# Performance work log

Measured on AMD Instinct MI355X. Metric: run time of the kernel, lower is better.

## Reference

```python
import jax, jax.numpy as jnp
import numpy as np

B, C, H, W = 16, 256, 32, 32
N_HEAD, DIM_HEAD = 8, 32  # dim_hidden = 256 == C


def setup_inputs() -> dict:
    key = jax.random.key(0)
    ks = jax.random.split(key, 9)
    s = 1.0 / np.sqrt(C)
    return {
        "x": jax.random.normal(ks[0], (B, C, H, W), dtype=jnp.float32),
        "w_q": jax.random.normal(ks[1], (C, C), dtype=jnp.float32) * s,
        "b_q": jnp.zeros((C,), dtype=jnp.float32),
        "w_k": jax.random.normal(ks[2], (C, C), dtype=jnp.float32) * s,
        "b_k": jnp.zeros((C,), dtype=jnp.float32),
        "w_v": jax.random.normal(ks[3], (C, C), dtype=jnp.float32) * s,
        "b_v": jnp.zeros((C,), dtype=jnp.float32),
        "w_o": jax.random.normal(ks[4], (C, C), dtype=jnp.float32) * s,
        "b_o": jnp.zeros((C,), dtype=jnp.float32),
    }


def reference(x, w_q, b_q, w_k, b_k, w_v, b_v, w_o, b_o):
    b, c, h, w = x.shape
    L = h * w
    scale = DIM_HEAD ** (-0.5)
    xf = x.reshape(b, c, L)  # [b, c, L]

    def proj(wm, bm):
        # 1x1 conv == per-position linear over channels
        y = jnp.einsum('oc,bcl->bol', wm, xf) + bm[None, :, None]
        return y.reshape(b, N_HEAD, DIM_HEAD, L)

    q = proj(w_q, b_q) * scale
    k = proj(w_k, b_k)
    v = proj(w_v, b_v)

    sim = jnp.einsum('bndl,bndm->bnlm', q, k)           # [b, n, L, L]
    att = jax.nn.softmax(sim, axis=-1)
    out = jnp.einsum('bnlm,bndm->bndl', att, v)         # [b, n, d, L]
    out = out.reshape(b, c, L)
    out = jnp.einsum('oc,bcl->bol', w_o, out) + b_o[None, :, None]
    return out.reshape(b, c, h, w)
```

## Files before the change

### kernel.cpp

```cpp
#include <hip/hip_runtime.h>
#include <hip/hip_bf16.h>
#include <math.h>

namespace {
constexpr int B_ = 16, C_ = 256, L_ = 1024, NH_ = 8, DH_ = 32;

typedef __attribute__((ext_vector_type(8))) short short8v;
typedef __attribute__((ext_vector_type(4))) float float4v;

__device__ __forceinline__ short f2bf(float f) {
    unsigned u = __builtin_bit_cast(unsigned, f);
    u += 0x7fffu + ((u >> 16) & 1u);
    return (short)(u >> 16);
}
__device__ __forceinline__ float bf2f(short s) {
    unsigned u = ((unsigned)(unsigned short)s) << 16;
    return __builtin_bit_cast(float, u);
}
__device__ __forceinline__ unsigned pkrn(float a, float b) {
    float2 f; f.x = a; f.y = b;
    __hip_bfloat162 h = __float22bfloat162_rn(f);
    unsigned u;
    __builtin_memcpy(&u, &h, sizeof(u));
    return u;
}
__device__ __forceinline__ void gld16(const short* g, short* l) {
    __builtin_amdgcn_global_load_lds(
        (const __attribute__((address_space(1))) unsigned*)g,
        (__attribute__((address_space(3))) unsigned*)l, 16, 0, 0);
}

__global__ __launch_bounds__(256) void xpose_kernel(
    const float* __restrict__ x, short* __restrict__ xthi)
{
    const int lt = blockIdx.x, ct = blockIdx.y, b = blockIdx.z;
    const int t = threadIdx.x;
    __shared__ float sX[64][68];

#pragma unroll
    for (int e = 0; e < 4; ++e) {
        const int row = e * 16 + (t >> 4);
        const int col = (t & 15) * 4;
        float4 v = *(const float4*)&x[((size_t)b * C_ + ct * 64 + row) * L_ + lt * 64 + col];
        *(float4*)&sX[row][col] = v;
    }
    __syncthreads();

    const int l = t & 63, cg = t >> 6;
    short hi[16];
#pragma unroll
    for (int i = 0; i < 16; ++i) hi[i] = f2bf(sX[cg * 16 + i][l]);
    const size_t base = ((size_t)b * L_ + lt * 64 + l) * C_ + ct * 64 + cg * 16;
    *(short8v*)&xthi[base]     = *(short8v*)&hi[0];
    *(short8v*)&xthi[base + 8] = *(short8v*)&hi[8];
}

__global__ __launch_bounds__(256) void stackw_kernel(
    const float* __restrict__ wq, const float* __restrict__ wk,
    const float* __restrict__ wv, const float* __restrict__ wo,
    short* __restrict__ WA, short* __restrict__ WoA)
{
    const int g = blockIdx.x * 256 + threadIdx.x;
    if (g < 768 * 256) {
        const int o = g >> 8, cc = g & 255;
        const float* src = (o < 256) ? wq : (o < 512) ? wk : wv;
        const float v = src[(size_t)(o & 255) * 256 + cc];
        const short hi = f2bf(v);
        const short lo = f2bf(v - bf2f(hi));
        WA[(size_t)o * 512 + cc]       = hi;
        WA[(size_t)o * 512 + 256 + cc] = lo;
    } else {
        const int g2 = g - 768 * 256;
        const int o = g2 >> 8, cc = g2 & 255;
        const float v = wo[(size_t)o * 256 + cc];
        const short hi = f2bf(v);
        const short lo = f2bf(v - bf2f(hi));
        WoA[(size_t)o * 512 + cc]       = hi;
        WoA[(size_t)o * 512 + 256 + cc] = lo;
    }
}

template <int KTOT, int EPI>
__global__ __launch_bounds__(256, 3) void gemm_kernel(
    const short* __restrict__ A, const short* __restrict__ B0,
    const float* __restrict__ bias0, const float* __restrict__ bias1, const float* __restrict__ bias2,
    float qscale, void* __restrict__ out0, void* __restrict__ out1, void* __restrict__ out2)
{
    const int lt = blockIdx.x, ot = blockIdx.y, b = blockIdx.z;
    const int t = threadIdx.x, wv = t >> 6, lane = t & 63;
    const int quad = lane >> 4, c = lane & 15;
    const int wo = (wv & 1) * 64, wl = (wv >> 1) * 64;

    __shared__ short sA[128 * 64];
    __shared__ short sB[128 * 64];

    float4v acc[4][4];
#pragma unroll
    for (int i = 0; i < 4; ++i)
#pragma unroll
        for (int j = 0; j < 4; ++j) acc[i][j] = (float4v)0.f;

    const short* Arow = A + (size_t)(ot * 128) * KTOT;
    const int srow = t >> 3, sseg = t & 7;
    const int seg = sseg ^ (srow & 7);

    for (int kk = 0; kk < KTOT / 64; ++kk) {
        __syncthreads();
#pragma unroll
        for (int e = 0; e < 4; ++e) {
            gld16(Arow + (size_t)(e * 32 + srow) * KTOT + kk * 64 + seg * 8,
                  &sA[(e * 256 + t) * 8]);
            gld16(B0 + ((size_t)b * L_ + lt * 128 + e * 32 + srow) * 256 + (kk & 3) * 64 + seg * 8,
                  &sB[(e * 256 + t) * 8]);
        }
        __syncthreads();

#pragma unroll
        for (int kc2 = 0; kc2 < 2; ++kc2) {
            short8v af[4], bf[4];
#pragma unroll
            for (int i = 0; i < 4; ++i) {
                const int row = wo + 16 * i + c;
                af[i] = *(const short8v*)&sA[row * 64 + (((kc2 * 4 + quad) ^ (c & 7)) * 8)];
            }
#pragma unroll
            for (int j = 0; j < 4; ++j) {
                const int row = wl + 16 * j + c;
                bf[j] = *(const short8v*)&sB[row * 64 + (((kc2 * 4 + quad) ^ (c & 7)) * 8)];
            }
#pragma unroll
            for (int i = 0; i < 4; ++i)
#pragma unroll
                for (int j = 0; j < 4; ++j)
                    acc[i][j] = __builtin_amdgcn_mfma_f32_16x16x32_bf16(af[i], bf[j], acc[i][j], 0, 0, 0);
        }
    }

    if constexpr (EPI == 0) {
        const int typ = ot >> 1;
        const int chbase = (ot & 1) * 128 + wo;
        const float* bp = (typ == 0) ? bias0 : (typ == 1) ? bias1 : bias2;
        const float sc = (typ == 0) ? qscale : 1.f;
        short* outp = (short*)((typ == 0) ? out0 : (typ == 1) ? out1 : out2);
        if (typ < 2) {
#pragma unroll
            for (int i = 0; i < 4; ++i) {
                const int ch0 = chbase + 16 * i + quad * 4;
                const int head = ch0 >> 5, d0 = ch0 & 31;
                float bias[4];
#pragma unroll
                for (int r = 0; r < 4; ++r) bias[r] = bp[ch0 + r];
#pragma unroll
                for (int j = 0; j < 4; ++j) {
                    const int l = lt * 128 + wl + 16 * j + c;
                    short4 sv;
                    sv.x = f2bf((acc[i][j][0] + bias[0]) * sc);
                    sv.y = f2bf((acc[i][j][1] + bias[1]) * sc);
                    sv.z = f2bf((acc[i][j][2] + bias[2]) * sc);
                    sv.w = f2bf((acc[i][j][3] + bias[3]) * sc);
                    *(short4*)&outp[(((size_t)b * NH_ + head) * L_ + l) * 32 + d0] = sv;
                }
            }
        } else {
#pragma unroll
            for (int i = 0; i < 4; ++i)
#pragma unroll
                for (int r = 0; r < 4; ++r) {
                    const int ch = chbase + 16 * i + quad * 4 + r;
                    const float bias = bp[ch];
#pragma unroll
                    for (int j = 0; j < 4; ++j)
                        outp[((size_t)b * C_ + ch) * L_ + lt * 128 + wl + 16 * j + c] =
                            f2bf(acc[i][j][r] + bias);
                }
        }
    } else {
        float* outp = (float*)out0;
#pragma unroll
        for (int i = 0; i < 4; ++i)
#pragma unroll
            for (int r = 0; r < 4; ++r) {
                const int ch = ot * 128 + wo + 16 * i + quad * 4 + r;
                const float bias = bias0[ch];
#pragma unroll
                for (int j = 0; j < 4; ++j)
                    outp[((size_t)b * C_ + ch) * L_ + lt * 128 + wl + 16 * j + c] =
                        acc[i][j][r] + bias;
            }
    }
}

__global__ __launch_bounds__(256, 4) void attn_kernel(
    const short* __restrict__ qt,
    const short* __restrict__ kt,
    const short* __restrict__ vb,
    short* __restrict__ athi)
{
    const int flat = blockIdx.x;
    const int g = ((flat >> 6) << 3) | (flat & 7);
    const int chunk = (flat >> 3) & 7;
    const int b = g >> 3, h = g & 7;
    const int t = threadIdx.x;
    const int wv = t >> 6, lane = t & 63;
    const int quad = lane >> 4, c = lane & 15;
    const int lq0 = chunk * 128 + wv * 32;

    __shared__ __align__(16) short sK[2][64 * 32];
    __shared__ __align__(16) short sV[2][2][32 * 32];
    __shared__ __align__(16) short sPT[4][2][16][72];

    const size_t bh = (size_t)b * NH_ + h;
    const short* qbase = qt + (bh * L_) * 32;
    const short* kbase = kt + (bh * L_) * 32;
    const size_t vrow = (size_t)b * C_ + h * DH_;

    short8v qfrag[2];
#pragma unroll
    for (int qf = 0; qf < 2; ++qf)
        qfrag[qf] = *(const short8v*)(qbase + (size_t)(lq0 + qf * 16 + c) * 32 + quad * 8);

    float lp4[2][4];
#pragma unroll
    for (int qf = 0; qf < 2; ++qf)
#pragma unroll
        for (int r = 0; r < 4; ++r) lp4[qf][r] = 0.f;
    float4v o_acc[2][2];
#pragma unroll
    for (int qf = 0; qf < 2; ++qf) { o_acc[qf][0] = (float4v)0.f; o_acc[qf][1] = (float4v)0.f; }

    auto stage = [&](int m0, int buf) {
        gld16(kbase + (size_t)(m0 + (t >> 2)) * 32 + (t & 3) * 8, &sK[buf][t * 8]);
        gld16(vb + (vrow + ((t >> 2) & 31)) * L_ + m0 + (t >> 7) * 32 + (t & 3) * 8,
              (short*)sV[buf] + t * 8);
    };

    stage(0, 0);

    for (int i = 0; i < 16; ++i) {
        __syncthreads();
        if (i < 15) stage((i + 1) * 64, (i + 1) & 1);
        const int buf = i & 1;

        short8v kf[4], vf[2][2];
#pragma unroll
        for (int kb = 0; kb < 4; ++kb)
            kf[kb] = *(const short8v*)&sK[buf][(kb * 16 + c) * 32 + quad * 8];
#pragma unroll
        for (int kc = 0; kc < 2; ++kc)
#pragma unroll
            for (int nb2 = 0; nb2 < 2; ++nb2)
                vf[kc][nb2] = *(const short8v*)&sV[buf][kc][(nb2 * 16 + c) * 32 + quad * 8];

        float4v st[2][4];
#pragma unroll
        for (int qf = 0; qf < 2; ++qf)
#pragma unroll
            for (int kb = 0; kb < 4; ++kb)
                st[qf][kb] = __builtin_amdgcn_mfma_f32_16x16x32_bf16(kf[kb], qfrag[qf], (float4v)0.f, 0, 0, 0);

#pragma unroll
        for (int qf = 0; qf < 2; ++qf)
#pragma unroll
            for (int kb = 0; kb < 4; ++kb) {
                float p[4];
#pragma unroll
                for (int r = 0; r < 4; ++r) {
                    p[r] = __builtin_amdgcn_exp2f(st[qf][kb][r]);
                    lp4[qf][r] += p[r];
                }
                uint2 w;
                w.x = pkrn(p[0], p[1]);
                w.y = pkrn(p[2], p[3]);
                *(uint2*)&sPT[wv][qf][c][kb * 16 + quad * 4] = w;
            }

#pragma unroll
        for (int qf = 0; qf < 2; ++qf)
#pragma unroll
            for (int kc = 0; kc < 2; ++kc) {
                const short8v pf = *(const short8v*)&sPT[wv][qf][c][kc * 32 + quad * 8];
#pragma unroll
                for (int nb2 = 0; nb2 < 2; ++nb2)
                    o_acc[qf][nb2] = __builtin_amdgcn_mfma_f32_16x16x32_bf16(vf[kc][nb2], pf, o_acc[qf][nb2], 0, 0, 0);
            }
    }

#pragma unroll
    for (int qf = 0; qf < 2; ++qf) {
        float l = (lp4[qf][0] + lp4[qf][1]) + (lp4[qf][2] + lp4[qf][3]);
        l += __shfl_xor(l, 16);
        l += __shfl_xor(l, 32);
        const float inv = 1.f / l;
#pragma unroll
        for (int nb2 = 0; nb2 < 2; ++nb2) {
            short4 sv;
            sv.x = f2bf(o_acc[qf][nb2][0] * inv);
            sv.y = f2bf(o_acc[qf][nb2][1] * inv);
            sv.z = f2bf(o_acc[qf][nb2][2] * inv);
            sv.w = f2bf(o_acc[qf][nb2][3] * inv);
            *(short4*)&athi[((size_t)b * L_ + lq0 + qf * 16 + c) * C_ + h * DH_ + nb2 * 16 + quad * 4] = sv;
        }
    }
}

}

extern "C" void kernel_launch(void* const* d_in, const int* in_sizes, int n_in,
                              void* d_out, int out_size, void* d_ws, size_t ws_size,
                              hipStream_t stream) {
    const float* x   = (const float*)d_in[0];
    const float* w_q = (const float*)d_in[1];
    const float* b_q = (const float*)d_in[2];
    const float* w_k = (const float*)d_in[3];
    const float* b_k = (const float*)d_in[4];
    const float* w_v = (const float*)d_in[5];
    const float* b_v = (const float*)d_in[6];
    const float* w_o = (const float*)d_in[7];
    const float* b_o = (const float*)d_in[8];
    float* out = (float*)d_out;

    const size_t NT = (size_t)B_ * L_ * C_;
    short* xthi = (short*)d_ws;
    short* WA   = xthi + NT;
    short* WoA  = WA + 768 * 512;
    short* qt   = WoA + 256 * 512;
    short* kt   = qt + NT;
    short* vb   = kt + NT;
    short* athi = vb + NT;

    const float scale_q = 0.17677669529663687f * 1.4426950408889634f;

    xpose_kernel<<<dim3(L_ / 64, C_ / 64, B_), 256, 0, stream>>>(x, xthi);
    stackw_kernel<<<dim3(1024), 256, 0, stream>>>(w_q, w_k, w_v, w_o, WA, WoA);
    gemm_kernel<512, 0><<<dim3(L_ / 128, 6, B_), 256, 0, stream>>>(
        WA, xthi, b_q, b_k, b_v, scale_q, qt, kt, vb);
    attn_kernel<<<dim3(1024), 256, 0, stream>>>(qt, kt, vb, athi);
    gemm_kernel<512, 1><<<dim3(L_ / 128, 2, B_), 256, 0, stream>>>(
        WoA, athi, b_o, nullptr, nullptr, 1.f, out, nullptr, nullptr);
}
```

Baseline: 151.3 us.

## Fuse x transpose/convert into QKV GEMM and software-pipeline attention PV step

Removes the separate transpose kernel: the QKV GEMM now reads fp32 x directly, converts it to bf16 and writes it transposed into padded shared memory. This saves one write and one read of a bf16 copy of x plus a kernel launch. The attention kernel is restructured so the P·V MFMA of the previous tile overlaps the QK/exp of the current one. It does this with a double-buffered, XOR-swizzled P buffer and single-buffered K/V with two barriers per step. The trade-offs are non-async global loads in the GEMM, which redo the conversion once per output tile, and extra synchronisation in attention.

```diff
diff --git a/kernel.cpp b/kernel.cpp
--- a/kernel.cpp
+++ b/kernel.cpp
@@ -28,31 +28,6 @@
     __builtin_amdgcn_global_load_lds(
         (const __attribute__((address_space(1))) unsigned*)g,
         (__attribute__((address_space(3))) unsigned*)l, 16, 0, 0);
-}
-
-__global__ __launch_bounds__(256) void xpose_kernel(
-    const float* __restrict__ x, short* __restrict__ xthi)
-{
-    const int lt = blockIdx.x, ct = blockIdx.y, b = blockIdx.z;
-    const int t = threadIdx.x;
-    __shared__ float sX[64][68];
-
-#pragma unroll
-    for (int e = 0; e < 4; ++e) {
-        const int row = e * 16 + (t >> 4);
-        const int col = (t & 15) * 4;
-        float4 v = *(const float4*)&x[((size_t)b * C_ + ct * 64 + row) * L_ + lt * 64 + col];
-        *(float4*)&sX[row][col] = v;
-    }
-    __syncthreads();
-
-    const int l = t & 63, cg = t >> 6;
-    short hi[16];
-#pragma unroll
-    for (int i = 0; i < 16; ++i) hi[i] = f2bf(sX[cg * 16 + i][l]);
-    const size_t base = ((size_t)b * L_ + lt * 64 + l) * C_ + ct * 64 + cg * 16;
-    *(short8v*)&xthi[base]     = *(short8v*)&hi[0];
-    *(short8v*)&xthi[base + 8] = *(short8v*)&hi[8];
 }
 
 __global__ __launch_bounds__(256) void stackw_kernel(
@@ -80,9 +55,9 @@
     }
 }
 
-template <int KTOT, int EPI>
+template <int EPI>
 __global__ __launch_bounds__(256, 3) void gemm_kernel(
-    const short* __restrict__ A, const short* __restrict__ B0,
+    const short* __restrict__ A, const short* __restrict__ Bt, const float* __restrict__ Bx,
     const float* __restrict__ bias0, const float* __restrict__ bias1, const float* __restrict__ bias2,
     float qscale, void* __restrict__ out0, void* __restrict__ out1, void* __restrict__ out2)
 {
@@ -92,7 +67,7 @@
     const int wo = (wv & 1) * 64, wl = (wv >> 1) * 64;
 
     __shared__ short sA[128 * 64];
-    __shared__ short sB[128 * 64];
+    __shared__ short sB[128 * 72];
 
     float4v acc[4][4];
 #pragma unroll
@@ -100,18 +75,38 @@
 #pragma unroll
         for (int j = 0; j < 4; ++j) acc[i][j] = (float4v)0.f;
 
-    const short* Arow = A + (size_t)(ot * 128) * KTOT;
+    const short* Arow = A + (size_t)(ot * 128) * 512;
     const int srow = t >> 3, sseg = t & 7;
     const int seg = sseg ^ (srow & 7);
 
-    for (int kk = 0; kk < KTOT / 64; ++kk) {
+    for (int kk = 0; kk < 8; ++kk) {
         __syncthreads();
 #pragma unroll
-        for (int e = 0; e < 4; ++e) {
-            gld16(Arow + (size_t)(e * 32 + srow) * KTOT + kk * 64 + seg * 8,
+        for (int e = 0; e < 4; ++e)
+            gld16(Arow + (size_t)(e * 32 + srow) * 512 + kk * 64 + seg * 8,
                   &sA[(e * 256 + t) * 8]);
-            gld16(B0 + ((size_t)b * L_ + lt * 128 + e * 32 + srow) * 256 + (kk & 3) * 64 + seg * 8,
-                  &sB[(e * 256 + t) * 8]);
+        if constexpr (EPI == 0) {
+            const int cchunk = (kk & 3) * 64;
+            const int ll0 = (t & 31) * 4;
+            const int cs  = (t >> 5) * 8;
+            float4 xv[8];
+#pragma unroll
+            for (int cc = 0; cc < 8; ++cc)
+                xv[cc] = *(const float4*)&Bx[((size_t)b * C_ + cchunk + cs + cc) * L_ + lt * 128 + ll0];
+#pragma unroll
+            for (int i = 0; i < 4; ++i) {
+                uint4 w;
+                w.x = pkrn(((const float*)&xv[0])[i], ((const float*)&xv[1])[i]);
+                w.y = pkrn(((const float*)&xv[2])[i], ((const float*)&xv[3])[i]);
+                w.z = pkrn(((const float*)&xv[4])[i], ((const float*)&xv[5])[i]);
+                w.w = pkrn(((const float*)&xv[6])[i], ((const float*)&xv[7])[i]);
+                *(uint4*)&sB[(ll0 + i) * 72 + cs] = w;
+            }
+        } else {
+#pragma unroll
+            for (int e = 0; e < 4; ++e)
+                gld16(Bt + ((size_t)b * L_ + lt * 128 + e * 32 + srow) * 256 + (kk & 3) * 64 + seg * 8,
+                      &sB[(e * 256 + t) * 8]);
         }
         __syncthreads();
 
@@ -126,7 +121,10 @@
 #pragma unroll
             for (int j = 0; j < 4; ++j) {
                 const int row = wl + 16 * j + c;
-                bf[j] = *(const short8v*)&sB[row * 64 + (((kc2 * 4 + quad) ^ (c & 7)) * 8)];
+                if constexpr (EPI == 0)
+                    bf[j] = *(const short8v*)&sB[row * 72 + (kc2 * 4 + quad) * 8];
+                else
+                    bf[j] = *(const short8v*)&sB[row * 64 + (((kc2 * 4 + quad) ^ (c & 7)) * 8)];
             }
 #pragma unroll
             for (int i = 0; i < 4; ++i)
@@ -205,9 +203,9 @@
     const int quad = lane >> 4, c = lane & 15;
     const int lq0 = chunk * 128 + wv * 32;
 
-    __shared__ __align__(16) short sK[2][64 * 32];
-    __shared__ __align__(16) short sV[2][2][32 * 32];
-    __shared__ __align__(16) short sPT[4][2][16][72];
+    __shared__ __align__(16) short sK[64 * 32];
+    __shared__ __align__(16) short sV[2][32 * 32];
+    __shared__ __align__(16) short sPT[2][4][2][16][64];
 
     const size_t bh = (size_t)b * NH_ + h;
     const short* qbase = qt + (bh * L_) * 32;
@@ -228,61 +226,75 @@
 #pragma unroll
     for (int qf = 0; qf < 2; ++qf) { o_acc[qf][0] = (float4v)0.f; o_acc[qf][1] = (float4v)0.f; }
 
-    auto stage = [&](int m0, int buf) {
-        gld16(kbase + (size_t)(m0 + (t >> 2)) * 32 + (t & 3) * 8, &sK[buf][t * 8]);
+    auto stage = [&](int m0) {
+        gld16(kbase + (size_t)(m0 + (t >> 2)) * 32 + (t & 3) * 8, &sK[t * 8]);
         gld16(vb + (vrow + ((t >> 2) & 31)) * L_ + m0 + (t >> 7) * 32 + (t & 3) * 8,
-              (short*)sV[buf] + t * 8);
+              (short*)sV + t * 8);
     };
 
-    stage(0, 0);
-
-    for (int i = 0; i < 16; ++i) {
-        __syncthreads();
-        if (i < 15) stage((i + 1) * 64, (i + 1) & 1);
-        const int buf = i & 1;
-
-        short8v kf[4], vf[2][2];
-#pragma unroll
-        for (int kb = 0; kb < 4; ++kb)
-            kf[kb] = *(const short8v*)&sK[buf][(kb * 16 + c) * 32 + quad * 8];
-#pragma unroll
-        for (int kc = 0; kc < 2; ++kc)
-#pragma unroll
-            for (int nb2 = 0; nb2 < 2; ++nb2)
-                vf[kc][nb2] = *(const short8v*)&sV[buf][kc][(nb2 * 16 + c) * 32 + quad * 8];
-
-        float4v st[2][4];
-#pragma unroll
-        for (int qf = 0; qf < 2; ++qf)
+    stage(0);
+
+    short8v vf[2][2], vfp[2][2];
+
+#pragma unroll
+    for (int i = 0; i <= 16; ++i) {
+        short8v kf[4];
+        if (i < 16) {
+            __syncthreads();
 #pragma unroll
             for (int kb = 0; kb < 4; ++kb)
-                st[qf][kb] = __builtin_amdgcn_mfma_f32_16x16x32_bf16(kf[kb], qfrag[qf], (float4v)0.f, 0, 0, 0);
-
-#pragma unroll
-        for (int qf = 0; qf < 2; ++qf)
-#pragma unroll
-            for (int kb = 0; kb < 4; ++kb) {
-                float p[4];
-#pragma unroll
-                for (int r = 0; r < 4; ++r) {
-                    p[r] = __builtin_amdgcn_exp2f(st[qf][kb][r]);
-                    lp4[qf][r] += p[r];
+                kf[kb] = *(const short8v*)&sK[(kb * 16 + c) * 32 + quad * 8];
+#pragma unroll
+            for (int kc = 0; kc < 2; ++kc)
+#pragma unroll
+                for (int nb2 = 0; nb2 < 2; ++nb2)
+                    vf[kc][nb2] = *(const short8v*)&sV[kc][(nb2 * 16 + c) * 32 + quad * 8];
+            __syncthreads();
+            if (i < 15) stage((i + 1) * 64);
+        }
+
+        if (i > 0) {
+            const int pb = (i - 1) & 1;
+#pragma unroll
+            for (int qf = 0; qf < 2; ++qf)
+#pragma unroll
+                for (int kc = 0; kc < 2; ++kc) {
+                    const int G = (kc * 4 + quad) ^ (c & 7);
+                    const short8v pf = *(const short8v*)&sPT[pb][wv][qf][c][G * 8];
+#pragma unroll
+                    for (int nb2 = 0; nb2 < 2; ++nb2)
+                        o_acc[qf][nb2] = __builtin_amdgcn_mfma_f32_16x16x32_bf16(vfp[kc][nb2], pf, o_acc[qf][nb2], 0, 0, 0);
                 }
-                uint2 w;
-                w.x = pkrn(p[0], p[1]);
-                w.y = pkrn(p[2], p[3]);
-                *(uint2*)&sPT[wv][qf][c][kb * 16 + quad * 4] = w;
-            }
-
-#pragma unroll
-        for (int qf = 0; qf < 2; ++qf)
-#pragma unroll
-            for (int kc = 0; kc < 2; ++kc) {
-                const short8v pf = *(const short8v*)&sPT[wv][qf][c][kc * 32 + quad * 8];
-#pragma unroll
-                for (int nb2 = 0; nb2 < 2; ++nb2)
-                    o_acc[qf][nb2] = __builtin_amdgcn_mfma_f32_16x16x32_bf16(vf[kc][nb2], pf, o_acc[qf][nb2], 0, 0, 0);
-            }
+        }
+
+        if (i < 16) {
+            float4v st[2][4];
+#pragma unroll
+            for (int qf = 0; qf < 2; ++qf)
+#pragma unroll
+                for (int kb = 0; kb < 4; ++kb)
+                    st[qf][kb] = __builtin_amdgcn_mfma_f32_16x16x32_bf16(kf[kb], qfrag[qf], (float4v)0.f, 0, 0, 0);
+#pragma unroll
+            for (int qf = 0; qf < 2; ++qf)
+#pragma unroll
+                for (int kb = 0; kb < 4; ++kb) {
+                    float p[4];
+#pragma unroll
+                    for (int r = 0; r < 4; ++r) {
+                        p[r] = __builtin_amdgcn_exp2f(st[qf][kb][r]);
+                        lp4[qf][r] += p[r];
+                    }
+                    uint2 w;
+                    w.x = pkrn(p[0], p[1]);
+                    w.y = pkrn(p[2], p[3]);
+                    const int Gw = (kb * 2 + (quad >> 1)) ^ (c & 7);
+                    *(uint2*)&sPT[i & 1][wv][qf][c][Gw * 8 + (quad & 1) * 4] = w;
+                }
+#pragma unroll
+            for (int kc = 0; kc < 2; ++kc)
+#pragma unroll
+                for (int nb2 = 0; nb2 < 2; ++nb2) vfp[kc][nb2] = vf[kc][nb2];
+        }
     }
 
 #pragma unroll
@@ -320,8 +332,7 @@
     float* out = (float*)d_out;
 
     const size_t NT = (size_t)B_ * L_ * C_;
-    short* xthi = (short*)d_ws;
-    short* WA   = xthi + NT;
+    short* WA   = (short*)d_ws;
     short* WoA  = WA + 768 * 512;
     short* qt   = WoA + 256 * 512;
     short* kt   = qt + NT;
@@ -330,11 +341,10 @@
 
     const float scale_q = 0.17677669529663687f * 1.4426950408889634f;
 
-    xpose_kernel<<<dim3(L_ / 64, C_ / 64, B_), 256, 0, stream>>>(x, xthi);
     stackw_kernel<<<dim3(1024), 256, 0, stream>>>(w_q, w_k, w_v, w_o, WA, WoA);
-    gemm_kernel<512, 0><<<dim3(L_ / 128, 6, B_), 256, 0, stream>>>(
-        WA, xthi, b_q, b_k, b_v, scale_q, qt, kt, vb);
+    gemm_kernel<0><<<dim3(L_ / 128, 6, B_), 256, 0, stream>>>(
+        WA, nullptr, x, b_q, b_k, b_v, scale_q, qt, kt, vb);
     attn_kernel<<<dim3(1024), 256, 0, stream>>>(qt, kt, vb, athi);
-    gemm_kernel<512, 1><<<dim3(L_ / 128, 2, B_), 256, 0, stream>>>(
-        WoA, athi, b_o, nullptr, nullptr, 1.f, out, nullptr, nullptr);
-}
+    gemm_kernel<1><<<dim3(L_ / 128, 2, B_), 256, 0, stream>>>(
+        WoA, athi, nullptr, b_o, nullptr, nullptr, 1.f, out, nullptr, nullptr);
+}
```

Measured after the change: 372.0 us. 2.46x slower.

## Software-pipeline PV MFMA one step behind QK and swizzle P tile in LDS

Applied to the files above, without the earlier changes.

Restructures the attention loop so the P·V MFMAs for the previous key block run while the current block's QK MFMAs and exp are computed. P is double-buffered in LDS and the V fragments are carried over in registers. K/V staging drops to a single buffer, with two barriers per iteration around the fragment loads. The P tile drops its padding and uses an XOR swizzle to avoid bank conflicts. The intent is to overlap the exp/VALU work with MFMA and cut LDS footprint, at the cost of an extra barrier and more live registers.

```diff
diff --git a/kernel.cpp b/kernel.cpp
--- a/kernel.cpp
+++ b/kernel.cpp
@@ -205,9 +205,9 @@
     const int quad = lane >> 4, c = lane & 15;
     const int lq0 = chunk * 128 + wv * 32;
 
-    __shared__ __align__(16) short sK[2][64 * 32];
-    __shared__ __align__(16) short sV[2][2][32 * 32];
-    __shared__ __align__(16) short sPT[4][2][16][72];
+    __shared__ __align__(16) short sK[64 * 32];
+    __shared__ __align__(16) short sV[2][32 * 32];
+    __shared__ __align__(16) short sPT[2][4][2][16][64];
 
     const size_t bh = (size_t)b * NH_ + h;
     const short* qbase = qt + (bh * L_) * 32;
@@ -228,61 +228,75 @@
 #pragma unroll
     for (int qf = 0; qf < 2; ++qf) { o_acc[qf][0] = (float4v)0.f; o_acc[qf][1] = (float4v)0.f; }
 
-    auto stage = [&](int m0, int buf) {
-        gld16(kbase + (size_t)(m0 + (t >> 2)) * 32 + (t & 3) * 8, &sK[buf][t * 8]);
+    auto stage = [&](int m0) {
+        gld16(kbase + (size_t)(m0 + (t >> 2)) * 32 + (t & 3) * 8, &sK[t * 8]);
         gld16(vb + (vrow + ((t >> 2) & 31)) * L_ + m0 + (t >> 7) * 32 + (t & 3) * 8,
-              (short*)sV[buf] + t * 8);
+              (short*)sV + t * 8);
     };
 
-    stage(0, 0);
-
-    for (int i = 0; i < 16; ++i) {
-        __syncthreads();
-        if (i < 15) stage((i + 1) * 64, (i + 1) & 1);
-        const int buf = i & 1;
-
+    stage(0);
+
+    short8v vfp[2][2];
+
+    for (int i = 0; i <= 16; ++i) {
         short8v kf[4], vf[2][2];
-#pragma unroll
-        for (int kb = 0; kb < 4; ++kb)
-            kf[kb] = *(const short8v*)&sK[buf][(kb * 16 + c) * 32 + quad * 8];
-#pragma unroll
-        for (int kc = 0; kc < 2; ++kc)
-#pragma unroll
-            for (int nb2 = 0; nb2 < 2; ++nb2)
-                vf[kc][nb2] = *(const short8v*)&sV[buf][kc][(nb2 * 16 + c) * 32 + quad * 8];
-
-        float4v st[2][4];
-#pragma unroll
-        for (int qf = 0; qf < 2; ++qf)
+        if (i < 16) {
+            __syncthreads();
 #pragma unroll
             for (int kb = 0; kb < 4; ++kb)
-                st[qf][kb] = __builtin_amdgcn_mfma_f32_16x16x32_bf16(kf[kb], qfrag[qf], (float4v)0.f, 0, 0, 0);
-
-#pragma unroll
-        for (int qf = 0; qf < 2; ++qf)
-#pragma unroll
-            for (int kb = 0; kb < 4; ++kb) {
-                float p[4];
-#pragma unroll
-                for (int r = 0; r < 4; ++r) {
-                    p[r] = __builtin_amdgcn_exp2f(st[qf][kb][r]);
-                    lp4[qf][r] += p[r];
+                kf[kb] = *(const short8v*)&sK[(kb * 16 + c) * 32 + quad * 8];
+#pragma unroll
+            for (int kc = 0; kc < 2; ++kc)
+#pragma unroll
+                for (int nb2 = 0; nb2 < 2; ++nb2)
+                    vf[kc][nb2] = *(const short8v*)&sV[kc][(nb2 * 16 + c) * 32 + quad * 8];
+            __syncthreads();
+            if (i < 15) stage((i + 1) * 64);
+        }
+
+        if (i > 0) {
+            const int pb = (i - 1) & 1;
+#pragma unroll
+            for (int qf = 0; qf < 2; ++qf)
+#pragma unroll
+                for (int kc = 0; kc < 2; ++kc) {
+                    const int G = (kc * 4 + quad) ^ (c & 7);
+                    const short8v pf = *(const short8v*)&sPT[pb][wv][qf][c][G * 8];
+#pragma unroll
+                    for (int nb2 = 0; nb2 < 2; ++nb2)
+                        o_acc[qf][nb2] = __builtin_amdgcn_mfma_f32_16x16x32_bf16(vfp[kc][nb2], pf, o_acc[qf][nb2], 0, 0, 0);
                 }
-                uint2 w;
-                w.x = pkrn(p[0], p[1]);
-                w.y = pkrn(p[2], p[3]);
-                *(uint2*)&sPT[wv][qf][c][kb * 16 + quad * 4] = w;
-            }
-
-#pragma unroll
-        for (int qf = 0; qf < 2; ++qf)
-#pragma unroll
-            for (int kc = 0; kc < 2; ++kc) {
-                const short8v pf = *(const short8v*)&sPT[wv][qf][c][kc * 32 + quad * 8];
-#pragma unroll
-                for (int nb2 = 0; nb2 < 2; ++nb2)
-                    o_acc[qf][nb2] = __builtin_amdgcn_mfma_f32_16x16x32_bf16(vf[kc][nb2], pf, o_acc[qf][nb2], 0, 0, 0);
-            }
+        }
+
+        if (i < 16) {
+            const int cb = i & 1;
+            float4v st[2][4];
+#pragma unroll
+            for (int qf = 0; qf < 2; ++qf)
+#pragma unroll
+                for (int kb = 0; kb < 4; ++kb)
+                    st[qf][kb] = __builtin_amdgcn_mfma_f32_16x16x32_bf16(kf[kb], qfrag[qf], (float4v)0.f, 0, 0, 0);
+#pragma unroll
+            for (int qf = 0; qf < 2; ++qf)
+#pragma unroll
+                for (int kb = 0; kb < 4; ++kb) {
+                    float p[4];
+#pragma unroll
+                    for (int r = 0; r < 4; ++r) {
+                        p[r] = __builtin_amdgcn_exp2f(st[qf][kb][r]);
+                        lp4[qf][r] += p[r];
+                    }
+                    uint2 w;
+                    w.x = pkrn(p[0], p[1]);
+                    w.y = pkrn(p[2], p[3]);
+                    const int Gw = (kb * 2 + (quad >> 1)) ^ (c & 7);
+                    *(uint2*)&sPT[cb][wv][qf][c][Gw * 8 + (quad & 1) * 4] = w;
+                }
+#pragma unroll
+            for (int kc = 0; kc < 2; ++kc)
+#pragma unroll
+                for (int nb2 = 0; nb2 < 2; ++nb2) vfp[kc][nb2] = vf[kc][nb2];
+        }
     }
 
 #pragma unroll
```

New measurement: 148.5 us. Within noise of the previous version (-1.8%).
